# Kernel tuning notes

Hardware: AMD Instinct MI355X
Metric: run time of the kernel (lower is better)

The kernel has to match this reference:

```python
import jax, jax.numpy as jnp
import numpy as np

B, H, W = 16, 512, 512  # mask resolution; feature maps are 2H x 2W


def setup_inputs() -> dict:
    key = jax.random.key(0)
    k0, k1, k2, k3, k4 = jax.random.split(key, 5)
    mask = jax.random.uniform(k0, (B, 2, H, W), dtype=jnp.float32)
    xl_out = jax.random.normal(k1, (B, 3, 2 * H, 2 * W), dtype=jnp.float32)
    yl_out = jax.random.normal(k2, (B, 3, 2 * H, 2 * W), dtype=jnp.float32)
    conv_w = jax.random.normal(k3, (3, 3), dtype=jnp.float32) * 0.1  # 1x1 conv [out_c, in_c]
    conv_b = jax.random.normal(k4, (3,), dtype=jnp.float32) * 0.1
    return {"mask": mask, "xl_out": xl_out, "yl_out": yl_out,
            "conv_w": conv_w, "conv_b": conv_b}


def reference(mask, xl_out, yl_out, conv_w, conv_b):
    b, _, h, w = mask.shape
    up = jax.image.resize(mask, (b, 2, 2 * h, 2 * w), method="bilinear")  # [B,2,2H,2W]
    x_mask = up[:, 0:1]  # [B,1,2H,2W]
    y_mask = up[:, 1:2]
    fused = x_mask * xl_out + y_mask * yl_out  # [B,3,2H,2W]
    # 1x1 conv == channel mixing matmul, then ReLU.
    out = jnp.einsum("oi,bihw->bohw", conv_w, fused) + conv_b[None, :, None, None]
    out = jax.nn.relu(out)
    return (out, x_mask, y_mask)
```

## Files before the change

### kernel.cpp

```cpp
#include <hip/hip_runtime.h>

#define BATCH 16
#define HIN   512
#define WIN   512
#define HOUT  1024
#define WOUT  1024

#define OUT_ELEMS   ((size_t)BATCH * 3 * HOUT * WOUT)
#define MASK_ELEMS  ((size_t)BATCH * HOUT * WOUT)

__global__ __launch_bounds__(256) void fused_upsample_conv_kernel(
    const float* __restrict__ mask,
    const float* __restrict__ xl,
    const float* __restrict__ yl,
    const float* __restrict__ cw,
    const float* __restrict__ cb,
    float* __restrict__ out)
{
    const int oh = blockIdx.x;
    const int b  = blockIdx.y;
    const int tx = threadIdx.x;
    const int ow0 = tx * 4;

    const int r = oh >> 1;
    int rA, rB; float wyA, wyB;
    if (oh & 1) { rA = r;                  rB = (r + 1 < HIN) ? r + 1 : HIN - 1; wyA = 0.75f; wyB = 0.25f; }
    else        { rA = (r > 0) ? r - 1 : 0; rB = r;                              wyA = 0.25f; wyB = 0.75f; }

    const int t2 = tx * 2;
    const int cM = (t2 > 0) ? t2 - 1 : 0;
    const int c0 = t2;
    const int c1 = t2 + 1;
    const int c2 = (t2 + 2 < WIN) ? t2 + 2 : WIN - 1;

    const size_t mplane = (size_t)HIN * WIN;
    const float* m0A = mask + ((size_t)b * 2 + 0) * mplane + (size_t)rA * WIN;
    const float* m0B = mask + ((size_t)b * 2 + 0) * mplane + (size_t)rB * WIN;
    const float* m1A = mask + ((size_t)b * 2 + 1) * mplane + (size_t)rA * WIN;
    const float* m1B = mask + ((size_t)b * 2 + 1) * mplane + (size_t)rB * WIN;

    float v0[4], v1[4];
    const int cols[4] = {cM, c0, c1, c2};
#pragma unroll
    for (int j = 0; j < 4; ++j) {
        v0[j] = wyA * m0A[cols[j]] + wyB * m0B[cols[j]];
        v1[j] = wyA * m1A[cols[j]] + wyB * m1B[cols[j]];
    }

    float4 xm, ym;
    xm.x = 0.25f*v0[0] + 0.75f*v0[1];
    xm.y = 0.75f*v0[1] + 0.25f*v0[2];
    xm.z = 0.25f*v0[1] + 0.75f*v0[2];
    xm.w = 0.75f*v0[2] + 0.25f*v0[3];
    ym.x = 0.25f*v1[0] + 0.75f*v1[1];
    ym.y = 0.75f*v1[1] + 0.25f*v1[2];
    ym.z = 0.25f*v1[1] + 0.75f*v1[2];
    ym.w = 0.75f*v1[2] + 0.25f*v1[3];

    const float w00 = cw[0], w01 = cw[1], w02 = cw[2];
    const float w10 = cw[3], w11 = cw[4], w12 = cw[5];
    const float w20 = cw[6], w21 = cw[7], w22 = cw[8];
    const float b0 = cb[0], b1 = cb[1], b2 = cb[2];

    const size_t oplane = (size_t)HOUT * WOUT;
    const size_t rowoff = (size_t)oh * WOUT + ow0;

    const float4 x0 = *(const float4*)(xl + ((size_t)b * 3 + 0) * oplane + rowoff);
    const float4 x1 = *(const float4*)(xl + ((size_t)b * 3 + 1) * oplane + rowoff);
    const float4 x2 = *(const float4*)(xl + ((size_t)b * 3 + 2) * oplane + rowoff);
    const float4 y0 = *(const float4*)(yl + ((size_t)b * 3 + 0) * oplane + rowoff);
    const float4 y1 = *(const float4*)(yl + ((size_t)b * 3 + 1) * oplane + rowoff);
    const float4 y2 = *(const float4*)(yl + ((size_t)b * 3 + 2) * oplane + rowoff);

    float4 f0, f1, f2;
    f0.x = xm.x*x0.x + ym.x*y0.x;  f0.y = xm.y*x0.y + ym.y*y0.y;
    f0.z = xm.z*x0.z + ym.z*y0.z;  f0.w = xm.w*x0.w + ym.w*y0.w;
    f1.x = xm.x*x1.x + ym.x*y1.x;  f1.y = xm.y*x1.y + ym.y*y1.y;
    f1.z = xm.z*x1.z + ym.z*y1.z;  f1.w = xm.w*x1.w + ym.w*y1.w;
    f2.x = xm.x*x2.x + ym.x*y2.x;  f2.y = xm.y*x2.y + ym.y*y2.y;
    f2.z = xm.z*x2.z + ym.z*y2.z;  f2.w = xm.w*x2.w + ym.w*y2.w;

    float4 o0, o1, o2;
    o0.x = fmaxf(w00*f0.x + w01*f1.x + w02*f2.x + b0, 0.0f);
    o0.y = fmaxf(w00*f0.y + w01*f1.y + w02*f2.y + b0, 0.0f);
    o0.z = fmaxf(w00*f0.z + w01*f1.z + w02*f2.z + b0, 0.0f);
    o0.w = fmaxf(w00*f0.w + w01*f1.w + w02*f2.w + b0, 0.0f);
    o1.x = fmaxf(w10*f0.x + w11*f1.x + w12*f2.x + b1, 0.0f);
    o1.y = fmaxf(w10*f0.y + w11*f1.y + w12*f2.y + b1, 0.0f);
    o1.z = fmaxf(w10*f0.z + w11*f1.z + w12*f2.z + b1, 0.0f);
    o1.w = fmaxf(w10*f0.w + w11*f1.w + w12*f2.w + b1, 0.0f);
    o2.x = fmaxf(w20*f0.x + w21*f1.x + w22*f2.x + b2, 0.0f);
    o2.y = fmaxf(w20*f0.y + w21*f1.y + w22*f2.y + b2, 0.0f);
    o2.z = fmaxf(w20*f0.z + w21*f1.z + w22*f2.z + b2, 0.0f);
    o2.w = fmaxf(w20*f0.w + w21*f1.w + w22*f2.w + b2, 0.0f);

    *(float4*)(out + ((size_t)b * 3 + 0) * oplane + rowoff) = o0;
    *(float4*)(out + ((size_t)b * 3 + 1) * oplane + rowoff) = o1;
    *(float4*)(out + ((size_t)b * 3 + 2) * oplane + rowoff) = o2;
    *(float4*)(out + OUT_ELEMS + (size_t)b * oplane + rowoff) = xm;
    *(float4*)(out + OUT_ELEMS + MASK_ELEMS + (size_t)b * oplane + rowoff) = ym;
}

extern "C" void kernel_launch(void* const* d_in, const int* in_sizes, int n_in,
                              void* d_out, int out_size, void* d_ws, size_t ws_size,
                              hipStream_t stream) {
    const float* mask = (const float*)d_in[0];
    const float* xl   = (const float*)d_in[1];
    const float* yl   = (const float*)d_in[2];
    const float* cw   = (const float*)d_in[3];
    const float* cb   = (const float*)d_in[4];
    float* out = (float*)d_out;

    dim3 grid(HOUT, BATCH);
    dim3 block(256);
    fused_upsample_conv_kernel<<<grid, block, 0, stream>>>(mask, xl, yl, cw, cb, out);
}
```

Measured before the change: 592.4 us.

## Process two output rows per block with 8-wide vectors and nontemporal loads/stores

After: 658.9 us. +11.2%, slower.

```diff
diff --git a/kernel.cpp b/kernel.cpp
--- a/kernel.cpp
+++ b/kernel.cpp
@@ -9,6 +9,8 @@
 #define OUT_ELEMS   ((size_t)BATCH * 3 * HOUT * WOUT)
 #define MASK_ELEMS  ((size_t)BATCH * HOUT * WOUT)
 
+typedef float f32x4 __attribute__((ext_vector_type(4)));
+
 __global__ __launch_bounds__(256) void fused_upsample_conv_kernel(
     const float* __restrict__ mask,
     const float* __restrict__ xl,
@@ -17,88 +19,103 @@
     const float* __restrict__ cb,
     float* __restrict__ out)
 {
-    const int oh = blockIdx.x;
-    const int b  = blockIdx.y;
-    const int tx = threadIdx.x;
-    const int ow0 = tx * 4;
+    const int k    = blockIdx.x;
+    const int b    = blockIdx.y;
+    const int tid  = threadIdx.x;
+    const int half = tid >> 7;
+    const int u    = tid & 127;
+    const int oh   = 2 * k + half;
 
-    const int r = oh >> 1;
-    int rA, rB; float wyA, wyB;
-    if (oh & 1) { rA = r;                  rB = (r + 1 < HIN) ? r + 1 : HIN - 1; wyA = 0.75f; wyB = 0.25f; }
-    else        { rA = (r > 0) ? r - 1 : 0; rB = r;                              wyA = 0.25f; wyB = 0.75f; }
+    int rA, rB; float wA, wB;
+    if (half == 0) { rA = (k > 0) ? k - 1 : 0;       rB = k;  wA = 0.25f; wB = 0.75f; }
+    else           { rA = k; rB = (k + 1 < HIN) ? k + 1 : HIN - 1; wA = 0.75f; wB = 0.25f; }
 
-    const int t2 = tx * 2;
-    const int cM = (t2 > 0) ? t2 - 1 : 0;
-    const int c0 = t2;
-    const int c1 = t2 + 1;
-    const int c2 = (t2 + 2 < WIN) ? t2 + 2 : WIN - 1;
+    const int c0 = u * 4;
+    const int cm = (c0 > 0) ? c0 - 1 : 0;
+    const int cp = (c0 + 4 < WIN) ? c0 + 4 : WIN - 1;
 
     const size_t mplane = (size_t)HIN * WIN;
-    const float* m0A = mask + ((size_t)b * 2 + 0) * mplane + (size_t)rA * WIN;
-    const float* m0B = mask + ((size_t)b * 2 + 0) * mplane + (size_t)rB * WIN;
-    const float* m1A = mask + ((size_t)b * 2 + 1) * mplane + (size_t)rA * WIN;
-    const float* m1B = mask + ((size_t)b * 2 + 1) * mplane + (size_t)rB * WIN;
+    const float* mA0 = mask + ((size_t)b * 2 + 0) * mplane + (size_t)rA * WIN;
+    const float* mB0 = mask + ((size_t)b * 2 + 0) * mplane + (size_t)rB * WIN;
+    const float* mA1 = mask + ((size_t)b * 2 + 1) * mplane + (size_t)rA * WIN;
+    const float* mB1 = mask + ((size_t)b * 2 + 1) * mplane + (size_t)rB * WIN;
 
-    float v0[4], v1[4];
-    const int cols[4] = {cM, c0, c1, c2};
+    const f32x4 A40 = *(const f32x4*)(mA0 + c0);
+    const f32x4 B40 = *(const f32x4*)(mB0 + c0);
+    const f32x4 A41 = *(const f32x4*)(mA1 + c0);
+    const f32x4 B41 = *(const f32x4*)(mB1 + c0);
+    const float Am0 = mA0[cm], Bm0 = mB0[cm], Ap0 = mA0[cp], Bp0 = mB0[cp];
+    const float Am1 = mA1[cm], Bm1 = mB1[cm], Ap1 = mA1[cp], Bp1 = mB1[cp];
+
+    float vv0[6], vv1[6];
+    vv0[0] = wA * Am0 + wB * Bm0;
+    vv1[0] = wA * Am1 + wB * Bm1;
 #pragma unroll
     for (int j = 0; j < 4; ++j) {
-        v0[j] = wyA * m0A[cols[j]] + wyB * m0B[cols[j]];
-        v1[j] = wyA * m1A[cols[j]] + wyB * m1B[cols[j]];
+        vv0[j + 1] = wA * A40[j] + wB * B40[j];
+        vv1[j + 1] = wA * A41[j] + wB * B41[j];
+    }
+    vv0[5] = wA * Ap0 + wB * Bp0;
+    vv1[5] = wA * Ap1 + wB * Bp1;
+
+    float xm[8], ym[8];
+#pragma unroll
+    for (int m = 0; m < 4; ++m) {
+        xm[2 * m]     = 0.25f * vv0[m]     + 0.75f * vv0[m + 1];
+        xm[2 * m + 1] = 0.75f * vv0[m + 1] + 0.25f * vv0[m + 2];
+        ym[2 * m]     = 0.25f * vv1[m]     + 0.75f * vv1[m + 1];
+        ym[2 * m + 1] = 0.75f * vv1[m + 1] + 0.25f * vv1[m + 2];
     }
 
-    float4 xm, ym;
-    xm.x = 0.25f*v0[0] + 0.75f*v0[1];
-    xm.y = 0.75f*v0[1] + 0.25f*v0[2];
-    xm.z = 0.25f*v0[1] + 0.75f*v0[2];
-    xm.w = 0.75f*v0[2] + 0.25f*v0[3];
-    ym.x = 0.25f*v1[0] + 0.75f*v1[1];
-    ym.y = 0.75f*v1[1] + 0.25f*v1[2];
-    ym.z = 0.25f*v1[1] + 0.75f*v1[2];
-    ym.w = 0.75f*v1[2] + 0.25f*v1[3];
+    const size_t oplane = (size_t)HOUT * WOUT;
+    const size_t rowoff = (size_t)oh * WOUT + (size_t)u * 8;
 
-    const float w00 = cw[0], w01 = cw[1], w02 = cw[2];
-    const float w10 = cw[3], w11 = cw[4], w12 = cw[5];
-    const float w20 = cw[6], w21 = cw[7], w22 = cw[8];
-    const float b0 = cb[0], b1 = cb[1], b2 = cb[2];
+    f32x4 X[3][2], Y[3][2];
+#pragma unroll
+    for (int cc = 0; cc < 3; ++cc) {
+        const f32x4* px = (const f32x4*)(xl + ((size_t)b * 3 + cc) * oplane + rowoff);
+        const f32x4* py = (const f32x4*)(yl + ((size_t)b * 3 + cc) * oplane + rowoff);
+        X[cc][0] = __builtin_nontemporal_load(px);
+        X[cc][1] = __builtin_nontemporal_load(px + 1);
+        Y[cc][0] = __builtin_nontemporal_load(py);
+        Y[cc][1] = __builtin_nontemporal_load(py + 1);
+    }
 
-    const size_t oplane = (size_t)HOUT * WOUT;
-    const size_t rowoff = (size_t)oh * WOUT + ow0;
+    float f[3][8];
+#pragma unroll
+    for (int cc = 0; cc < 3; ++cc)
+#pragma unroll
+        for (int j = 0; j < 8; ++j)
+            f[cc][j] = xm[j] * X[cc][j >> 2][j & 3] + ym[j] * Y[cc][j >> 2][j & 3];
 
-    const float4 x0 = *(const float4*)(xl + ((size_t)b * 3 + 0) * oplane + rowoff);
-    const float4 x1 = *(const float4*)(xl + ((size_t)b * 3 + 1) * oplane + rowoff);
-    const float4 x2 = *(const float4*)(xl + ((size_t)b * 3 + 2) * oplane + rowoff);
-    const float4 y0 = *(const float4*)(yl + ((size_t)b * 3 + 0) * oplane + rowoff);
-    const float4 y1 = *(const float4*)(yl + ((size_t)b * 3 + 1) * oplane + rowoff);
-    const float4 y2 = *(const float4*)(yl + ((size_t)b * 3 + 2) * oplane + rowoff);
+    const float w0[3] = {cw[0], cw[1], cw[2]};
+    const float w1[3] = {cw[3], cw[4], cw[5]};
+    const float w2[3] = {cw[6], cw[7], cw[8]};
+    const float bb[3] = {cb[0], cb[1], cb[2]};
 
-    float4 f0, f1, f2;
-    f0.x = xm.x*x0.x + ym.x*y0.x;  f0.y = xm.y*x0.y + ym.y*y0.y;
-    f0.z = xm.z*x0.z + ym.z*y0.z;  f0.w = xm.w*x0.w + ym.w*y0.w;
-    f1.x = xm.x*x1.x + ym.x*y1.x;  f1.y = xm.y*x1.y + ym.y*y1.y;
-    f1.z = xm.z*x1.z + ym.z*y1.z;  f1.w = xm.w*x1.w + ym.w*y1.w;
-    f2.x = xm.x*x2.x + ym.x*y2.x;  f2.y = xm.y*x2.y + ym.y*y2.y;
-    f2.z = xm.z*x2.z + ym.z*y2.z;  f2.w = xm.w*x2.w + ym.w*y2.w;
+#pragma unroll
+    for (int o = 0; o < 3; ++o) {
+        const float* wo = (o == 0) ? w0 : (o == 1) ? w1 : w2;
+        f32x4 r0, r1;
+#pragma unroll
+        for (int j = 0; j < 8; ++j) {
+            float v = fmaxf(wo[0] * f[0][j] + wo[1] * f[1][j] + wo[2] * f[2][j] + bb[o], 0.0f);
+            if (j < 4) r0[j] = v; else r1[j - 4] = v;
+        }
+        f32x4* po = (f32x4*)(out + ((size_t)b * 3 + o) * oplane + rowoff);
+        __builtin_nontemporal_store(r0, po);
+        __builtin_nontemporal_store(r1, po + 1);
+    }
 
-    float4 o0, o1, o2;
-    o0.x = fmaxf(w00*f0.x + w01*f1.x + w02*f2.x + b0, 0.0f);
-    o0.y = fmaxf(w00*f0.y + w01*f1.y + w02*f2.y + b0, 0.0f);
-    o0.z = fmaxf(w00*f0.z + w01*f1.z + w02*f2.z + b0, 0.0f);
-    o0.w = fmaxf(w00*f0.w + w01*f1.w + w02*f2.w + b0, 0.0f);
-    o1.x = fmaxf(w10*f0.x + w11*f1.x + w12*f2.x + b1, 0.0f);
-    o1.y = fmaxf(w10*f0.y + w11*f1.y + w12*f2.y + b1, 0.0f);
-    o1.z = fmaxf(w10*f0.z + w11*f1.z + w12*f2.z + b1, 0.0f);
-    o1.w = fmaxf(w10*f0.w + w11*f1.w + w12*f2.w + b1, 0.0f);
-    o2.x = fmaxf(w20*f0.x + w21*f1.x + w22*f2.x + b2, 0.0f);
-    o2.y = fmaxf(w20*f0.y + w21*f1.y + w22*f2.y + b2, 0.0f);
-    o2.z = fmaxf(w20*f0.z + w21*f1.z + w22*f2.z + b2, 0.0f);
-    o2.w = fmaxf(w20*f0.w + w21*f1.w + w22*f2.w + b2, 0.0f);
-
-    *(float4*)(out + ((size_t)b * 3 + 0) * oplane + rowoff) = o0;
-    *(float4*)(out + ((size_t)b * 3 + 1) * oplane + rowoff) = o1;
-    *(float4*)(out + ((size_t)b * 3 + 2) * oplane + rowoff) = o2;
-    *(float4*)(out + OUT_ELEMS + (size_t)b * oplane + rowoff) = xm;
-    *(float4*)(out + OUT_ELEMS + MASK_ELEMS + (size_t)b * oplane + rowoff) = ym;
+    f32x4 xa, xb, ya, yb;
+#pragma unroll
+    for (int j = 0; j < 4; ++j) { xa[j] = xm[j]; xb[j] = xm[j + 4]; ya[j] = ym[j]; yb[j] = ym[j + 4]; }
+    f32x4* pxm = (f32x4*)(out + OUT_ELEMS + (size_t)b * oplane + rowoff);
+    f32x4* pym = (f32x4*)(out + OUT_ELEMS + MASK_ELEMS + (size_t)b * oplane + rowoff);
+    __builtin_nontemporal_store(xa, pxm);
+    __builtin_nontemporal_store(xb, pxm + 1);
+    __builtin_nontemporal_store(ya, pym);
+    __builtin_nontemporal_store(yb, pym + 1);
 }
 
 extern "C" void kernel_launch(void* const* d_in, const int* in_sizes, int n_in,
@@ -111,7 +128,7 @@
     const float* cb   = (const float*)d_in[4];
     float* out = (float*)d_out;
 
-    dim3 grid(HOUT, BATCH);
+    dim3 grid(HIN, BATCH);
     dim3 block(256);
     fused_upsample_conv_kernel<<<grid, block, 0, stream>>>(mask, xl, yl, cw, cb, out);
 }
```
